# Kernel tuning notes

Measured on AMD Instinct MI355X. Metric: run time of the kernel, lower is better.

## Reference

```python
import jax, jax.numpy as jnp
import numpy as np
from jax import lax

B, S, E, DF, H, L, V, T = 32, 512, 512, 2048, 8, 2, 30000, 12
START, STOP = 10, 11
NEG = -10000.0


def setup_inputs() -> dict:
    key = jax.random.key(0)
    ks = jax.random.split(key, 12)
    g = lambda i, shape, sc=0.02: jax.random.normal(ks[i], shape, jnp.float32) * sc
    trans = jax.random.normal(ks[9], (T, T), jnp.float32)
    trans = trans.at[START, :].set(NEG).at[:, STOP].set(NEG)
    return {
        "sentence": jax.random.randint(ks[0], (B, S), 0, V),
        "seq_len": jax.random.randint(ks[1], (B,), 1, S + 1),
        "tags": jax.random.randint(ks[2], (B, S), 0, 10),
        "emb": g(3, (V, E), 1.0),
        "attn_in_w": g(4, (L, 3 * E, E)), "attn_in_b": jnp.zeros((L, 3 * E)),
        "attn_out_w": g(5, (L, E, E)), "attn_out_b": jnp.zeros((L, E)),
        "ln1_g": jnp.ones((L, E)), "ln1_b": jnp.zeros((L, E)),
        "ln2_g": jnp.ones((L, E)), "ln2_b": jnp.zeros((L, E)),
        "ff1_w": g(6, (L, DF, E)), "ff1_b": jnp.zeros((L, DF)),
        "ff2_w": g(7, (L, E, DF)), "ff2_b": jnp.zeros((L, E)),
        "tag_w": g(8, (T, E)), "tag_b": jnp.zeros((T,)),
        "transitions": trans,
    }


def _ln(x, g, b):
    m = x.mean(-1, keepdims=True)
    v = ((x - m) ** 2).mean(-1, keepdims=True)
    return (x - m) / jnp.sqrt(v + 1e-5) * g + b


def _mha(x, w_in, b_in, w_out, b_out):
    b_, s_, e_ = x.shape
    d = e_ // H
    qkv = x @ w_in.T + b_in
    q, k, v = jnp.split(qkv, 3, axis=-1)
    split = lambda t: t.reshape(b_, s_, H, d).transpose(0, 2, 1, 3)
    q, k, v = split(q), split(k), split(v)
    att = jax.nn.softmax(jnp.einsum('bhqd,bhkd->bhqk', q, k) / np.sqrt(d).astype(np.float32), axis=-1)
    o = jnp.einsum('bhqk,bhkd->bhqd', att, v).transpose(0, 2, 1, 3).reshape(b_, s_, e_)
    return o @ w_out.T + b_out


def _forward_impl(sentence, seq_len, tags, emb, attn_in_w, attn_in_b, attn_out_w,
                  attn_out_b, ln1_g, ln1_b, ln2_g, ln2_b, ff1_w, ff1_b, ff2_w,
                  ff2_b, tag_w, tag_b, transitions):
    # Transformer encoder features (dropout in eval mode -> identity)
    x = emb[sentence]  # (B,S,E)
    for l in range(L):
        x = _ln(x + _mha(x, attn_in_w[l], attn_in_b[l], attn_out_w[l], attn_out_b[l]), ln1_g[l], ln1_b[l])
        h = jax.nn.relu(x @ ff1_w[l].T + ff1_b[l]) @ ff2_w[l].T + ff2_b[l]
        x = _ln(x + h, ln2_g[l], ln2_b[l])
    feats = x @ tag_w.T + tag_b  # (B,S,T)

    # CRF forward algorithm (log-semiring scan, masked by seq_len)
    alpha0 = jnp.full((B, T), NEG, feats.dtype).at[:, START].set(0.0)

    def step(alpha, xs):
        emit_t, t = xs  # emit_t: (B,T)
        new = emit_t + jax.nn.logsumexp(alpha[:, None, :] + transitions[None, :, :], axis=-1)
        return jnp.where((t < seq_len)[:, None], new, alpha), None

    alpha, _ = lax.scan(step, alpha0, (feats.transpose(1, 0, 2), jnp.arange(S)))
    fwd_score = jax.nn.logsumexp(alpha + transitions[STOP][None, :], axis=-1)  # (B,)

    # gold score (vectorized _score_sentence)
    tags_ext = jnp.concatenate([jnp.full((B, 1), START, tags.dtype), tags], axis=1)  # (B,S+1)
    mask = jnp.arange(S)[None, :] < seq_len[:, None]  # (B,S)
    trans_sc = jnp.where(mask, transitions[tags_ext[:, 1:], tags_ext[:, :-1]], 0.0).sum(-1)
    emit_sc = jnp.where(mask, jnp.take_along_axis(feats, tags[:, :, None], axis=2)[..., 0], 0.0).sum(-1)
    last_tag = jnp.take_along_axis(tags_ext, seq_len[:, None], axis=1)[:, 0]
    gold = trans_sc + emit_sc + transitions[STOP, last_tag]

    return jnp.mean(fwd_score - gold)


def reference(sentence, seq_len, tags, emb, attn_in_w, attn_in_b, attn_out_w,
              attn_out_b, ln1_g, ln1_b, ln2_g, ln2_b, ff1_w, ff1_b, ff2_w,
              ff2_b, tag_w, tag_b, transitions):
    return _forward_impl(sentence, seq_len, tags, emb, attn_in_w, attn_in_b,
                         attn_out_w, attn_out_b, ln1_g, ln1_b, ln2_g, ln2_b,
                         ff1_w, ff1_b, ff2_w, ff2_b, tag_w, tag_b, transitions)
```

## Files before the change

kernel.cpp:

```cpp
#include <hip/hip_runtime.h>
#include <hip/hip_bf16.h>

#define BB 32
#define SSZ 512
#define EE 512
#define DFF 2048
#define HH 8
#define LL 2
#define TT 12
#define START_TAG 10
#define STOP_TAG 11
#define CB 8
#define CM (CB * SSZ)
#define NCHUNK (BB / CB)
#define NBH (CB * HH)
#define NBH_ALL (BB * HH)
#define NCHK 8

typedef __hip_bfloat16 bf16;
typedef __attribute__((ext_vector_type(8))) short short8;
typedef __attribute__((ext_vector_type(4))) float f32x4;

__device__ __forceinline__ float b2f(bf16 x) { return __bfloat162float(x); }
__device__ __forceinline__ float ldw(const void* p, size_t i, bool isbf) {
  return isbf ? __bfloat162float(((const bf16*)p)[i]) : ((const float*)p)[i];
}

__device__ __forceinline__ void gl_lds16(const bf16* g, bf16* l) {
  __builtin_amdgcn_global_load_lds(
      (const __attribute__((address_space(1))) void*)g,
      (__attribute__((address_space(3))) void*)l, 16, 0, 0);
}

__device__ __forceinline__ void stg128(const bf16* __restrict__ G, int ldk,
                                       int row0, int col0, bf16* lds0,
                                       int w, int l) {
#pragma unroll
  for (int q = 0; q < 2; ++q) {
    int lr = q * 64 + w * 8 + (l >> 3);
    int gs = (l & 7) ^ (lr & 7);
    gl_lds16(G + (size_t)(row0 + lr) * ldk + col0 + gs * 8,
             lds0 + (q * 64 + w * 8) * 64);
  }
}

__device__ __forceinline__ short8 ldfrag(const bf16* T, int row, int gr) {
  return *(const short8*)&T[row * 64 + ((gr ^ (row & 7)) << 3)];
}

__global__ void k_detect(const void* trans, int* dflag) {
  if (threadIdx.x == 0) {
    const unsigned short* u = (const unsigned short*)trans;
    dflag[0] = (u[START_TAG * TT] == 0xC61C && u[START_TAG * TT + 1] == 0xC61C) ? 1 : 0;
  }
}

__global__ void k_cvt(const void* src, bf16* dst, long n, const int* dflag) {
  bool isbf = dflag[0] != 0;
  for (long i = (long)blockIdx.x * 256 + threadIdx.x; i < n; i += (long)gridDim.x * 256)
    dst[i] = __float2bfloat16(ldw(src, i, isbf));
}

__global__ void k_embed(const int* sent, const void* emb, bf16* xb, const int* dflag) {
  bool isbf = dflag[0] != 0;
  int tok = blockIdx.x;
  int v = sent[tok];
  bf16* xo = xb + (size_t)tok * EE;
  for (int i = threadIdx.x; i < EE; i += 256)
    xo[i] = __float2bfloat16(ldw(emb, (size_t)v * EE + i, isbf));
}

__global__ __launch_bounds__(512, 4) void k_mg128(
    const bf16* __restrict__ A, const bf16* __restrict__ W,
    const void* __restrict__ bias, size_t boff, bf16* __restrict__ Cb,
    bf16* __restrict__ vtout, int M, int N, int K, int relu,
    const int* __restrict__ dflag) {
  constexpr int BUFSZ = 16384;
  extern __shared__ __align__(16) bf16 Sh[];
  const bool isbf = dflag[0] != 0;
  const int tid = threadIdx.x;
  const int l = tid & 63;
  const int w = tid >> 6;
  const int wm = w >> 1, wn = w & 1;
  const int lrow = l & 15, lk = l >> 4;
  const int m0 = blockIdx.x * 128, n0 = blockIdx.y * 128;

  f32x4 acc[2][4];
#pragma unroll
  for (int i = 0; i < 2; ++i)
#pragma unroll
    for (int j = 0; j < 4; ++j) acc[i][j] = (f32x4){0.f, 0.f, 0.f, 0.f};

  const int NT = K >> 6;

#pragma unroll
  for (int p = 0; p < 2; ++p) {
    stg128(A, K, m0, p * 64, Sh + p * BUFSZ, w, l);
    stg128(W, K, n0, p * 64, Sh + p * BUFSZ + 8192, w, l);
  }
  asm volatile("s_waitcnt vmcnt(4)" ::: "memory");
  __builtin_amdgcn_sched_barrier(0);
  __builtin_amdgcn_s_barrier();

#pragma unroll 1
  for (int t = 0; t < NT; ++t) {
    bf16* Ab = Sh + (t & 1) * BUFSZ;
    bf16* Bb = Ab + 8192;
    const bool more = (t + 2 < NT);
    short8 bfr[2][4], a0[2], a1[2];
#pragma unroll
    for (int kb = 0; kb < 2; ++kb) {
#pragma unroll
      for (int nf = 0; nf < 4; ++nf)
        bfr[kb][nf] = ldfrag(Bb, wn * 64 + nf * 16 + lrow, kb * 4 + lk);
      a0[kb] = ldfrag(Ab, wm * 32 + lrow, kb * 4 + lk);
      a1[kb] = ldfrag(Ab, wm * 32 + 16 + lrow, kb * 4 + lk);
    }
    asm volatile("s_waitcnt lgkmcnt(0)" ::: "memory");
    __builtin_amdgcn_sched_barrier(0);
    __builtin_amdgcn_s_barrier();
    __builtin_amdgcn_sched_barrier(0);
    if (more) {
      stg128(A, K, m0, (t + 2) * 64, Ab, w, l);
      stg128(W, K, n0, (t + 2) * 64, Bb, w, l);
    }
    __builtin_amdgcn_s_setprio(1);
#pragma unroll
    for (int kb = 0; kb < 2; ++kb)
#pragma unroll
      for (int nf = 0; nf < 4; ++nf)
        acc[0][nf] = __builtin_amdgcn_mfma_f32_16x16x32_bf16(
            a0[kb], bfr[kb][nf], acc[0][nf], 0, 0, 0);
#pragma unroll
    for (int kb = 0; kb < 2; ++kb)
#pragma unroll
      for (int nf = 0; nf < 4; ++nf)
        acc[1][nf] = __builtin_amdgcn_mfma_f32_16x16x32_bf16(
            a1[kb], bfr[kb][nf], acc[1][nf], 0, 0, 0);
    __builtin_amdgcn_s_setprio(0);
    if (more) asm volatile("s_waitcnt vmcnt(4)" ::: "memory");
    else asm volatile("s_waitcnt vmcnt(0)" ::: "memory");
    __builtin_amdgcn_sched_barrier(0);
    __builtin_amdgcn_s_barrier();
  }

  const bool vpath = (vtout != nullptr) && (n0 >= 1024);
  if (!vpath) {
#pragma unroll
    for (int nf = 0; nf < 4; ++nf) {
      const int c = wn * 64 + nf * 16 + lrow;
      const float bia = ldw(bias, boff + n0 + c, isbf);
#pragma unroll
      for (int mf = 0; mf < 2; ++mf)
#pragma unroll
        for (int r = 0; r < 4; ++r) {
          const int row = wm * 32 + mf * 16 + lk * 4 + r;
          float v = acc[mf][nf][r] + bia;
          if (relu) v = fmaxf(v, 0.f);
          Sh[row * 128 + (c ^ (((row >> 2) & 7) << 4))] = __float2bfloat16(v);
        }
    }
    __syncthreads();
#pragma unroll
    for (int p = 0; p < 4; ++p) {
      const int row = p * 32 + (tid >> 4);
      const int g = tid & 15;
      *(uint4*)(Cb + (size_t)(m0 + row) * N + n0 + g * 8) =
          *(const uint4*)&Sh[row * 128 + ((g * 8) ^ (((row >> 2) & 7) << 4))];
    }
  } else {
    const int pos0 = m0 & 511;
    const int blb = (m0 >> 9) * 8;
#pragma unroll
    for (int nf = 0; nf < 4; ++nf) {
      const int c = wn * 64 + nf * 16 + lrow;
      const float bia = ldw(bias, boff + n0 + c, isbf);
#pragma unroll
      for (int mf = 0; mf < 2; ++mf)
#pragma unroll
        for (int r = 0; r < 4; ++r) {
          const int row = wm * 32 + mf * 16 + lk * 4 + r;
          Sh[c * 128 + (row ^ (((c >> 2) & 7) << 4))] =
              __float2bfloat16(acc[mf][nf][r] + bia);
        }
    }
    __syncthreads();
#pragma unroll
    for (int p = 0; p < 4; ++p) {
      const int cc = p * 32 + (tid >> 4);
      const int g = tid & 15;
      const int vc = n0 - 1024 + cc;
      *(uint4*)(vtout + ((size_t)(blb + (vc >> 6)) * 64 + (vc & 63)) * 512 +
                pos0 + g * 8) =
          *(const uint4*)&Sh[cc * 128 + ((g * 8) ^ (((cc >> 2) & 7) << 4))];
    }
  }
}

#define LDP 72
__global__ __launch_bounds__(512) void k_flash(const bf16* __restrict__ qkv,
                                               const bf16* __restrict__ vt,
                                               bf16* __restrict__ ctx) {
  extern __shared__ __align__(16) bf16 Fs[];
  const int bh = blockIdx.x;
  const int bl = bh >> 3, h = bh & 7;
  const int m0 = blockIdx.y * 256;
  const int tid = threadIdx.x;
  const int l = tid & 63;
  const int w = tid >> 6;
  const int lrow = l & 15, lk = l >> 4;

  bf16* Psw = Fs + 16384 + w * (32 * LDP);

  short8 qf[2][2];
  {
    const bf16* Qb = qkv + (size_t)(bl * SSZ + m0 + w * 32) * 1536 + h * 64;
#pragma unroll
    for (int mf = 0; mf < 2; ++mf)
#pragma unroll
      for (int kb = 0; kb < 2; ++kb)
        qf[mf][kb] = *(const short8*)(Qb + (size_t)(mf * 16 + lrow) * 1536 + kb * 32 + lk * 8);
  }

  f32x4 acc_o[2][4];
  float lsum[2][4];
#pragma unroll
  for (int mf = 0; mf < 2; ++mf) {
#pragma unroll
    for (int nf = 0; nf < 4; ++nf) acc_o[mf][nf] = (f32x4){0.f, 0.f, 0.f, 0.f};
#pragma unroll
    for (int r = 0; r < 4; ++r) lsum[mf][r] = 0.f;
  }

  const int srow = w * 8 + (l >> 3);
  const int gsw = (l & 7) ^ (srow & 7);
  const bf16* Ksrc = qkv + (size_t)(bl * SSZ + srow) * 1536 + 512 + h * 64 + gsw * 8;
  const bf16* Vsrc = vt + ((size_t)bh * 64 + srow) * SSZ + gsw * 8;
#define STAGE_KV(kt, b)                                                       \
  do {                                                                        \
    gl_lds16(Ksrc + (size_t)(kt)*64 * 1536, Fs + (b)*8192 + w * 512);         \
    gl_lds16(Vsrc + (kt)*64, Fs + (b)*8192 + 4096 + w * 512);                 \
  } while (0)

  STAGE_KV(0, 0);
  __syncthreads();

  for (int kt = 0; kt < 8; ++kt) {
    const int cur = kt & 1;
    if (kt < 7) STAGE_KV(kt + 1, cur ^ 1);
    const bf16* Ks = Fs + cur * 8192;
    const bf16* Vs = Ks + 4096;

    f32x4 s[2][4];
#pragma unroll
    for (int mf = 0; mf < 2; ++mf)
#pragma unroll
      for (int nf = 0; nf < 4; ++nf) s[mf][nf] = (f32x4){0.f, 0.f, 0.f, 0.f};
#pragma unroll
    for (int kb = 0; kb < 2; ++kb) {
      short8 bk[4];
#pragma unroll
      for (int nf = 0; nf < 4; ++nf)
        bk[nf] = ldfrag(Ks, nf * 16 + lrow, kb * 4 + lk);
#pragma unroll
      for (int mf = 0; mf < 2; ++mf)
#pragma unroll
        for (int nf = 0; nf < 4; ++nf)
          s[mf][nf] = __builtin_amdgcn_mfma_f32_16x16x32_bf16(qf[mf][kb], bk[nf],
                                                              s[mf][nf], 0, 0, 0);
    }
#pragma unroll
    for (int mf = 0; mf < 2; ++mf)
#pragma unroll
      for (int r = 0; r < 4; ++r) {
        float p0 = __expf(0.125f * s[mf][0][r]);
        float p1 = __expf(0.125f * s[mf][1][r]);
        float p2 = __expf(0.125f * s[mf][2][r]);
        float p3 = __expf(0.125f * s[mf][3][r]);
        s[mf][0][r] = p0; s[mf][1][r] = p1; s[mf][2][r] = p2; s[mf][3][r] = p3;
        lsum[mf][r] += (p0 + p1) + (p2 + p3);
      }
#pragma unroll
    for (int mf = 0; mf < 2; ++mf)
#pragma unroll
      for (int nf = 0; nf < 4; ++nf)
#pragma unroll
        for (int r = 0; r < 4; ++r)
          Psw[(mf * 16 + lk * 4 + r) * LDP + nf * 16 + lrow] =
              __float2bfloat16(s[mf][nf][r]);
#pragma unroll
    for (int kb = 0; kb < 2; ++kb) {
      short8 ap[2], bv[4];
#pragma unroll
      for (int mf = 0; mf < 2; ++mf)
        ap[mf] = *(const short8*)&Psw[(mf * 16 + lrow) * LDP + kb * 32 + lk * 8];
#pragma unroll
      for (int nf = 0; nf < 4; ++nf)
        bv[nf] = ldfrag(Vs, nf * 16 + lrow, kb * 4 + lk);
#pragma unroll
      for (int mf = 0; mf < 2; ++mf)
#pragma unroll
        for (int nf = 0; nf < 4; ++nf)
          acc_o[mf][nf] = __builtin_amdgcn_mfma_f32_16x16x32_bf16(ap[mf], bv[nf],
                                                                  acc_o[mf][nf], 0, 0, 0);
    }
    __syncthreads();
  }
#undef STAGE_KV
#pragma unroll
  for (int mf = 0; mf < 2; ++mf) {
#pragma unroll
    for (int r = 0; r < 4; ++r) {
      float ls = lsum[mf][r];
      ls += __shfl_xor(ls, 1, 64);
      ls += __shfl_xor(ls, 2, 64);
      ls += __shfl_xor(ls, 4, 64);
      ls += __shfl_xor(ls, 8, 64);
      float inv = 1.f / ls;
      int q = m0 + w * 32 + mf * 16 + lk * 4 + r;
#pragma unroll
      for (int nf = 0; nf < 4; ++nf)
        ctx[((size_t)(bl * SSZ + q)) * EE + h * 64 + nf * 16 + lrow] =
            __float2bfloat16(acc_o[mf][nf][r] * inv);
    }
  }
}

__global__ void k_ln_res(bf16* xb, const bf16* hb, const void* g,
                         const void* be, size_t goff, const int* dflag) {
  bool isbf = dflag[0] != 0;
  int tok = blockIdx.x, tid = threadIdx.x;
  size_t base = (size_t)tok * EE;
  float v0 = b2f(xb[base + tid]) + b2f(hb[base + tid]);
  float v1 = b2f(xb[base + tid + 256]) + b2f(hb[base + tid + 256]);
  float s = v0 + v1, ss = v0 * v0 + v1 * v1;
#pragma unroll
  for (int off = 32; off > 0; off >>= 1) {
    s += __shfl_down(s, off, 64);
    ss += __shfl_down(ss, off, 64);
  }
  __shared__ float ps[4], pss[4];
  __shared__ float mean_s, rstd_s;
  int w = tid >> 6;
  if ((tid & 63) == 0) { ps[w] = s; pss[w] = ss; }
  __syncthreads();
  if (tid == 0) {
    float S_ = ps[0] + ps[1] + ps[2] + ps[3];
    float SS_ = pss[0] + pss[1] + pss[2] + pss[3];
    float mu = S_ / (float)EE;
    float var = SS_ / (float)EE - mu * mu;
    mean_s = mu;
    rstd_s = rsqrtf(var + 1e-5f);
  }
  __syncthreads();
  float mu = mean_s, rs = rstd_s;
  float r0 = (v0 - mu) * rs * ldw(g, goff + tid, isbf) + ldw(be, goff + tid, isbf);
  float r1 = (v1 - mu) * rs * ldw(g, goff + tid + 256, isbf) + ldw(be, goff + tid + 256, isbf);
  xb[base + tid] = __float2bfloat16(r0);
  xb[base + tid + 256] = __float2bfloat16(r1);
}

__global__ void k_feats(const bf16* xb, const bf16* tgw, const void* tgb,
                        float* feats, const int* dflag) {
  bool isbf = dflag[0] != 0;
  int m = blockIdx.x * 4 + (threadIdx.x >> 6);
  int lane = threadIdx.x & 63;
  uint4 raw = *(const uint4*)(xb + (size_t)m * EE + lane * 8);
  const bf16* rb = (const bf16*)&raw;
  float xv[8];
#pragma unroll
  for (int j = 0; j < 8; ++j) xv[j] = b2f(rb[j]);
#pragma unroll
  for (int t = 0; t < TT; ++t) {
    uint4 wraw = *(const uint4*)(tgw + t * EE + lane * 8);
    const bf16* wb = (const bf16*)&wraw;
    float s = 0.f;
#pragma unroll
    for (int j = 0; j < 8; ++j) s += xv[j] * b2f(wb[j]);
#pragma unroll
    for (int off = 32; off > 0; off >>= 1) s += __shfl_down(s, off, 64);
    if (lane == 0) feats[(size_t)m * TT + t] = s + ldw(tgb, t, isbf);
  }
}

__global__ void k_crf1(const float* feats, const int* seq_len, const void* trans_in,
                       float* cmat, const int* dflag) {
  bool isbf = dflag[0] != 0;
  int c = blockIdx.x, b = blockIdx.y;
  int tid = threadIdx.x;
  __shared__ float tr[144];
  __shared__ float abuf[2][144];
  if (tid < 144) tr[tid] = ldw(trans_in, tid, isbf);
  bool act = tid < 144;
  int i = tid / 12, j = tid % 12;
  if (act) abuf[0][tid] = (i == j) ? 0.f : -1e30f;
  __syncthreads();
  float trrow[12];
  if (act) {
#pragma unroll
    for (int k = 0; k < 12; ++k) trrow[k] = tr[i * 12 + k];
  }
  int len = seq_len[b];
  int t0 = c * 64;
  int t1 = min(len, t0 + 64);
  int cur = 0;
  for (int t = t0; t < t1; ++t) {
    float nv = 0.f;
    if (act) {
      float m = -1e30f, v[12];
#pragma unroll
      for (int k = 0; k < 12; ++k) {
        v[k] = trrow[k] + abuf[cur][k * 12 + j];
        m = fmaxf(m, v[k]);
      }
      float s = 0.f;
#pragma unroll
      for (int k = 0; k < 12; ++k) s += __expf(v[k] - m);
      nv = feats[((size_t)b * SSZ + t) * TT + i] + m + __logf(s);
    }
    if (act) abuf[cur ^ 1][tid] = nv;
    __syncthreads();
    cur ^= 1;
  }
  if (act) cmat[((size_t)b * NCHK + c) * 144 + tid] = abuf[cur][tid];
}

__global__ void k_crf2(const float* cmat, const float* feats, const int* tags,
                       const int* seq_len, const void* trans_in, float* bscore,
                       const int* dflag) {
  bool isbf = dflag[0] != 0;
  int b = blockIdx.x;
  int tid = threadIdx.x;
  __shared__ float tr[144];
  __shared__ float tbuf[2][144];
  __shared__ float alpha_sh[12];
  if (tid < 144) tr[tid] = ldw(trans_in, tid, isbf);
  bool act = tid < 144;
  int i = tid / 12, j = tid % 12;
  if (act) tbuf[0][tid] = cmat[((size_t)b * NCHK) * 144 + tid];
  __syncthreads();
  int cur = 0;
  for (int c = 1; c < NCHK; ++c) {
    float nv = 0.f;
    if (act) {
      const float* Cc = cmat + ((size_t)b * NCHK + c) * 144;
      float m = -1e30f, v[12];
#pragma unroll
      for (int k = 0; k < 12; ++k) {
        v[k] = Cc[i * 12 + k] + tbuf[cur][k * 12 + j];
        m = fmaxf(m, v[k]);
      }
      float s = 0.f;
#pragma unroll
      for (int k = 0; k < 12; ++k) s += __expf(v[k] - m);
      nv = m + __logf(s);
    }
    if (act) tbuf[cur ^ 1][tid] = nv;
    __syncthreads();
    cur ^= 1;
  }
  if (tid < 12) {
    float m = -1e30f, v[12];
#pragma unroll
    for (int k = 0; k < 12; ++k) {
      float a0 = (k == START_TAG) ? 0.f : -10000.f;
      v[k] = tbuf[cur][tid * 12 + k] + a0;
      m = fmaxf(m, v[k]);
    }
    float s = 0.f;
#pragma unroll
    for (int k = 0; k < 12; ++k) s += __expf(v[k] - m);
    alpha_sh[tid] = m + __logf(s);
  }
  __syncthreads();
  if (tid < 64) {
    int lane = tid;
    int len = seq_len[b];
    float part = 0.f;
    for (int s = lane; s < len; s += 64) {
      int ct = tags[b * SSZ + s];
      int pv = (s == 0) ? START_TAG : tags[b * SSZ + s - 1];
      part += tr[ct * 12 + pv] + feats[((size_t)b * SSZ + s) * TT + ct];
    }
#pragma unroll
    for (int off = 32; off > 0; off >>= 1) part += __shfl_down(part, off, 64);
    if (lane == 0) {
      float m = -1e30f;
#pragma unroll
      for (int k = 0; k < 12; ++k) m = fmaxf(m, alpha_sh[k] + tr[STOP_TAG * 12 + k]);
      float s = 0.f;
#pragma unroll
      for (int k = 0; k < 12; ++k) s += __expf(alpha_sh[k] + tr[STOP_TAG * 12 + k] - m);
      float fwd = m + __logf(s);
      int last = tags[b * SSZ + len - 1];
      bscore[b] = fwd - (part + tr[STOP_TAG * 12 + last]);
    }
  }
}

__global__ void k_final(const float* bscore, float* out) {
  int tid = threadIdx.x;
  float v = (tid < BB) ? bscore[tid] : 0.f;
#pragma unroll
  for (int off = 32; off > 0; off >>= 1) v += __shfl_down(v, off, 64);
  if (tid == 0) out[0] = v / (float)BB;
}

extern "C" void kernel_launch(void* const* d_in, const int* in_sizes, int n_in,
                              void* d_out, int out_size, void* d_ws, size_t ws_size,
                              hipStream_t stream) {
  const int* sentence = (const int*)d_in[0];
  const int* seq_len = (const int*)d_in[1];
  const int* tags = (const int*)d_in[2];
  const void* emb = d_in[3];
  const void* attn_in_w = d_in[4];
  const void* attn_in_b = d_in[5];
  const void* attn_out_w = d_in[6];
  const void* attn_out_b = d_in[7];
  const void* ln1_g = d_in[8];
  const void* ln1_b = d_in[9];
  const void* ln2_g = d_in[10];
  const void* ln2_b = d_in[11];
  const void* ff1_w = d_in[12];
  const void* ff1_b = d_in[13];
  const void* ff2_w = d_in[14];
  const void* ff2_b = d_in[15];
  const void* tag_w = d_in[16];
  const void* tag_b = d_in[17];
  const void* transitions = d_in[18];

  static int attr_done = 0;
  if (!attr_done) {
    (void)hipFuncSetAttribute((const void*)&k_mg128,
                              hipFuncAttributeMaxDynamicSharedMemorySize, 65536);
    (void)hipFuncSetAttribute((const void*)&k_flash,
                              hipFuncAttributeMaxDynamicSharedMemorySize, 131072);
    attr_done = 1;
  }
  const int GLDS = 65536;
  const int FLDS = (16384 + 8 * 32 * LDP) * 2;

  const int M = BB * SSZ;
  const size_t WEL = (size_t)LL * 3 * EE * EE + (size_t)LL * EE * EE +
                     (size_t)LL * DFF * EE + (size_t)LL * EE * DFF + (size_t)TT * EE;

  size_t o = 0;
  size_t f_feats = o; o += (size_t)M * TT;
  size_t f_bsc = o; o += 64;
  size_t f_cmat = o; o += (size_t)BB * NCHK * 144;
  size_t f_dflag = o; o += 16;
  size_t f_xb = o; o += (size_t)M * EE / 2;
  size_t f_hb = o; o += (size_t)M * EE / 2;
  size_t f_ctxb = o; o += (size_t)M * EE / 2;
  size_t f_act = o; o += (size_t)M * DFF / 2;
  size_t f_vt = o; o += (size_t)NBH_ALL * 64 * SSZ / 2;
  size_t f_w = o; o += (WEL + 1) / 2 + 8;
  size_t need_full = o * 4;
  bool full = ws_size >= need_full;

  float* ws = (float*)d_ws;
  if (full) {
    float* feats = ws + f_feats;
    float* bsc = ws + f_bsc;
    float* cmat = ws + f_cmat;
    int* dflag = (int*)(ws + f_dflag);
    bf16* xb = (bf16*)(ws + f_xb);
    bf16* hb = (bf16*)(ws + f_hb);
    bf16* ctxb = (bf16*)(ws + f_ctxb);
    bf16* act = (bf16*)(ws + f_act);
    bf16* vt = (bf16*)(ws + f_vt);
    bf16* w_aiw = (bf16*)(ws + f_w);
    bf16* w_aow = w_aiw + (size_t)LL * 3 * EE * EE;
    bf16* w_f1 = w_aow + (size_t)LL * EE * EE;
    bf16* w_f2 = w_f1 + (size_t)LL * DFF * EE;
    bf16* w_tg = w_f2 + (size_t)LL * EE * DFF;

    k_detect<<<dim3(1), dim3(64), 0, stream>>>(transitions, dflag);
    k_cvt<<<dim3(1024), dim3(256), 0, stream>>>(attn_in_w, w_aiw, (long)LL * 3 * EE * EE, dflag);
    k_cvt<<<dim3(512), dim3(256), 0, stream>>>(attn_out_w, w_aow, (long)LL * EE * EE, dflag);
    k_cvt<<<dim3(1024), dim3(256), 0, stream>>>(ff1_w, w_f1, (long)LL * DFF * EE, dflag);
    k_cvt<<<dim3(1024), dim3(256), 0, stream>>>(ff2_w, w_f2, (long)LL * EE * DFF, dflag);
    k_cvt<<<dim3(24), dim3(256), 0, stream>>>(tag_w, w_tg, (long)TT * EE, dflag);
    k_embed<<<dim3(M), dim3(256), 0, stream>>>(sentence, emb, xb, dflag);

    for (int l = 0; l < LL; ++l) {
      k_mg128<<<dim3(M / 128, 12), dim3(512), GLDS, stream>>>(
          xb, w_aiw + (size_t)l * 3 * EE * EE, attn_in_b, (size_t)l * 3 * EE,
          act, vt, M, 3 * EE, EE, 0, dflag);
      k_flash<<<dim3(NBH_ALL, 2), dim3(512), FLDS, stream>>>(act, vt, ctxb);
      k_mg128<<<dim3(M / 128, 4), dim3(512), GLDS, stream>>>(
          ctxb, w_aow + (size_t)l * EE * EE, attn_out_b, (size_t)l * EE,
          hb, (bf16*)nullptr, M, EE, EE, 0, dflag);
      k_ln_res<<<dim3(M), dim3(256), 0, stream>>>(xb, hb, ln1_g, ln1_b,
                                                  (size_t)l * EE, dflag);
      k_mg128<<<dim3(M / 128, 16), dim3(512), GLDS, stream>>>(
          xb, w_f1 + (size_t)l * DFF * EE, ff1_b, (size_t)l * DFF,
          act, (bf16*)nullptr, M, DFF, EE, 1, dflag);
      k_mg128<<<dim3(M / 128, 4), dim3(512), GLDS, stream>>>(
          act, w_f2 + (size_t)l * EE * DFF, ff2_b, (size_t)l * EE,
          hb, (bf16*)nullptr, M, EE, DFF, 0, dflag);
      k_ln_res<<<dim3(M), dim3(256), 0, stream>>>(xb, hb, ln2_g, ln2_b,
                                                  (size_t)l * EE, dflag);
    }
    k_feats<<<dim3(M / 4), dim3(256), 0, stream>>>(xb, w_tg, tag_b, feats, dflag);
    k_crf1<<<dim3(NCHK, BB), dim3(192), 0, stream>>>(feats, seq_len, transitions, cmat, dflag);
    k_crf2<<<dim3(BB), dim3(192), 0, stream>>>(cmat, feats, tags, seq_len, transitions, bsc, dflag);
    k_final<<<dim3(1), dim3(64), 0, stream>>>(bsc, (float*)d_out);
  } else {
    float* feats = ws;
    float* bsc = feats + (size_t)M * TT;
    float* cmat = bsc + 64;
    int* dflag = (int*)(cmat + (size_t)BB * NCHK * 144 + 16);
    bf16* xb = (bf16*)(dflag + 16);
    bf16* hb = xb + (size_t)M * EE;
    bf16* qkvb = hb + (size_t)CM * EE;
    bf16* ctxb = qkvb + (size_t)CM * 1536;
    bf16* ffh = ctxb + (size_t)CM * EE;
    bf16* vt = ffh + (size_t)CM * DFF;
    bf16* w_aiw = vt + (size_t)NBH * 64 * SSZ;
    bf16* w_aow = w_aiw + (size_t)LL * 3 * EE * EE;
    bf16* w_f1 = w_aow + (size_t)LL * EE * EE;
    bf16* w_f2 = w_f1 + (size_t)LL * DFF * EE;
    bf16* w_tg = w_f2 + (size_t)LL * EE * DFF;

    k_detect<<<dim3(1), dim3(64), 0, stream>>>(transitions, dflag);
    k_cvt<<<dim3(1024), dim3(256), 0, stream>>>(attn_in_w, w_aiw, (long)LL * 3 * EE * EE, dflag);
    k_cvt<<<dim3(512), dim3(256), 0, stream>>>(attn_out_w, w_aow, (long)LL * EE * EE, dflag);
    k_cvt<<<dim3(1024), dim3(256), 0, stream>>>(ff1_w, w_f1, (long)LL * DFF * EE, dflag);
    k_cvt<<<dim3(1024), dim3(256), 0, stream>>>(ff2_w, w_f2, (long)LL * EE * DFF, dflag);
    k_cvt<<<dim3(24), dim3(256), 0, stream>>>(tag_w, w_tg, (long)TT * EE, dflag);
    k_embed<<<dim3(M), dim3(256), 0, stream>>>(sentence, emb, xb, dflag);

    for (int l = 0; l < LL; ++l) {
      for (int c = 0; c < NCHUNK; ++c) {
        bf16* xbc = xb + (size_t)c * CM * EE;
        k_mg128<<<dim3(CM / 128, 12), dim3(512), GLDS, stream>>>(
            xbc, w_aiw + (size_t)l * 3 * EE * EE, attn_in_b, (size_t)l * 3 * EE,
            qkvb, vt, CM, 3 * EE, EE, 0, dflag);
        k_flash<<<dim3(NBH, 2), dim3(512), FLDS, stream>>>(qkvb, vt, ctxb);
        k_mg128<<<dim3(CM / 128, 4), dim3(512), GLDS, stream>>>(
            ctxb, w_aow + (size_t)l * EE * EE, attn_out_b, (size_t)l * EE,
            hb, (bf16*)nullptr, CM, EE, EE, 0, dflag);
        k_ln_res<<<dim3(CM), dim3(256), 0, stream>>>(xbc, hb, ln1_g, ln1_b,
                                                     (size_t)l * EE, dflag);
        k_mg128<<<dim3(CM / 128, 16), dim3(512), GLDS, stream>>>(
            xbc, w_f1 + (size_t)l * DFF * EE, ff1_b, (size_t)l * DFF,
            ffh, (bf16*)nullptr, CM, DFF, EE, 1, dflag);
        k_mg128<<<dim3(CM / 128, 4), dim3(512), GLDS, stream>>>(
            ffh, w_f2 + (size_t)l * EE * DFF, ff2_b, (size_t)l * EE,
            hb, (bf16*)nullptr, CM, EE, DFF, 0, dflag);
        k_ln_res<<<dim3(CM), dim3(256), 0, stream>>>(xbc, hb, ln2_g, ln2_b,
                                                     (size_t)l * EE, dflag);
      }
    }
    k_feats<<<dim3(M / 4), dim3(256), 0, stream>>>(xb, w_tg, tag_b, feats, dflag);
    k_crf1<<<dim3(NCHK, BB), dim3(192), 0, stream>>>(feats, seq_len, transitions, cmat, dflag);
    k_crf2<<<dim3(BB), dim3(192), 0, stream>>>(cmat, feats, tags, seq_len, transitions, bsc, dflag);
    k_final<<<dim3(1), dim3(64), 0, stream>>>(bsc, (float*)d_out);
  }
}
```

Before: 673.9 us.

## Rework GEMM to 256-thread blocks with 64x64 warp tiles and simpler double buffering

The 128x128 GEMM tile now runs with 4 waves instead of 8, so each wave computes a 64x64 subtile with 16 accumulators and reuses each A/B fragment across more MFMAs. The pipeline moves from a 2-ahead prefetch with manual vmcnt waits to a 1-ahead double buffer synchronised with __syncthreads. The V-transpose epilogue writes 4-element vectors to LDS. In exchange, per-thread register pressure and the number of staging loads per thread both grow, and the shallower prefetch can expose more global-load latency.

```diff
diff --git a/kernel.cpp b/kernel.cpp
--- a/kernel.cpp
+++ b/kernel.cpp
@@ -32,20 +32,12 @@
       (__attribute__((address_space(3))) void*)l, 16, 0, 0);
 }
 
-__device__ __forceinline__ void stg128(const bf16* __restrict__ G, int ldk,
-                                       int row0, int col0, bf16* lds0,
-                                       int w, int l) {
-#pragma unroll
-  for (int q = 0; q < 2; ++q) {
-    int lr = q * 64 + w * 8 + (l >> 3);
-    int gs = (l & 7) ^ (lr & 7);
-    gl_lds16(G + (size_t)(row0 + lr) * ldk + col0 + gs * 8,
-             lds0 + (q * 64 + w * 8) * 64);
-  }
-}
-
 __device__ __forceinline__ short8 ldfrag(const bf16* T, int row, int gr) {
   return *(const short8*)&T[row * 64 + ((gr ^ (row & 7)) << 3)];
+}
+
+__device__ __forceinline__ int swz(int row, int col) {
+  return row * 128 + (col ^ (((row >> 2) & 7) * 16));
 }
 
 __global__ void k_detect(const void* trans, int* dflag) {
@@ -70,12 +62,11 @@
     xo[i] = __float2bfloat16(ldw(emb, (size_t)v * EE + i, isbf));
 }
 
-__global__ __launch_bounds__(512, 4) void k_mg128(
+__global__ __launch_bounds__(256, 2) void k_mg128(
     const bf16* __restrict__ A, const bf16* __restrict__ W,
     const void* __restrict__ bias, size_t boff, bf16* __restrict__ Cb,
     bf16* __restrict__ vtout, int M, int N, int K, int relu,
     const int* __restrict__ dflag) {
-  constexpr int BUFSZ = 16384;
   extern __shared__ __align__(16) bf16 Sh[];
   const bool isbf = dflag[0] != 0;
   const int tid = threadIdx.x;
@@ -85,114 +76,116 @@
   const int lrow = l & 15, lk = l >> 4;
   const int m0 = blockIdx.x * 128, n0 = blockIdx.y * 128;
 
-  f32x4 acc[2][4];
-#pragma unroll
-  for (int i = 0; i < 2; ++i)
+  const int srow = w * 8 + (l >> 3);
+  const bf16* aS[4];
+  const bf16* bS[4];
+#pragma unroll
+  for (int q = 0; q < 4; ++q) {
+    int r = q * 32 + srow;
+    int gs = (l & 7) ^ (r & 7);
+    aS[q] = A + (size_t)(m0 + r) * K + gs * 8;
+    bS[q] = W + (size_t)(n0 + r) * K + gs * 8;
+  }
+
+  f32x4 acc[4][4];
+#pragma unroll
+  for (int i = 0; i < 4; ++i)
 #pragma unroll
     for (int j = 0; j < 4; ++j) acc[i][j] = (f32x4){0.f, 0.f, 0.f, 0.f};
 
   const int NT = K >> 6;
 
-#pragma unroll
-  for (int p = 0; p < 2; ++p) {
-    stg128(A, K, m0, p * 64, Sh + p * BUFSZ, w, l);
-    stg128(W, K, n0, p * 64, Sh + p * BUFSZ + 8192, w, l);
-  }
-  asm volatile("s_waitcnt vmcnt(4)" ::: "memory");
-  __builtin_amdgcn_sched_barrier(0);
-  __builtin_amdgcn_s_barrier();
+#define STG(t, buf)                                                       \
+  do {                                                                    \
+    bf16* dA = Sh + (buf)*16384;                                          \
+    bf16* dB = dA + 8192;                                                 \
+    _Pragma("unroll") for (int q = 0; q < 4; ++q) {                       \
+      gl_lds16(aS[q] + (t)*64, dA + (q * 32 + w * 8) * 64);               \
+      gl_lds16(bS[q] + (t)*64, dB + (q * 32 + w * 8) * 64);               \
+    }                                                                     \
+  } while (0)
+
+  STG(0, 0);
+  __syncthreads();
 
 #pragma unroll 1
   for (int t = 0; t < NT; ++t) {
-    bf16* Ab = Sh + (t & 1) * BUFSZ;
-    bf16* Bb = Ab + 8192;
-    const bool more = (t + 2 < NT);
-    short8 bfr[2][4], a0[2], a1[2];
-#pragma unroll
-    for (int kb = 0; kb < 2; ++kb) {
+    if (t + 1 < NT) STG(t + 1, (t + 1) & 1);
+    __builtin_amdgcn_sched_barrier(0);
+    const bf16* Ab = Sh + (t & 1) * 16384;
+    const bf16* Bb = Ab + 8192;
+    short8 af[4][2], bq[4][2];
+#pragma unroll
+    for (int f = 0; f < 4; ++f)
+#pragma unroll
+      for (int kb = 0; kb < 2; ++kb) {
+        af[f][kb] = ldfrag(Ab, wm * 64 + f * 16 + lrow, kb * 4 + lk);
+        bq[f][kb] = ldfrag(Bb, wn * 64 + f * 16 + lrow, kb * 4 + lk);
+      }
+    __builtin_amdgcn_s_setprio(1);
+#pragma unroll
+    for (int mf = 0; mf < 4; ++mf)
 #pragma unroll
       for (int nf = 0; nf < 4; ++nf)
-        bfr[kb][nf] = ldfrag(Bb, wn * 64 + nf * 16 + lrow, kb * 4 + lk);
-      a0[kb] = ldfrag(Ab, wm * 32 + lrow, kb * 4 + lk);
-      a1[kb] = ldfrag(Ab, wm * 32 + 16 + lrow, kb * 4 + lk);
-    }
-    asm volatile("s_waitcnt lgkmcnt(0)" ::: "memory");
-    __builtin_amdgcn_sched_barrier(0);
-    __builtin_amdgcn_s_barrier();
-    __builtin_amdgcn_sched_barrier(0);
-    if (more) {
-      stg128(A, K, m0, (t + 2) * 64, Ab, w, l);
-      stg128(W, K, n0, (t + 2) * 64, Bb, w, l);
-    }
-    __builtin_amdgcn_s_setprio(1);
-#pragma unroll
-    for (int kb = 0; kb < 2; ++kb)
-#pragma unroll
-      for (int nf = 0; nf < 4; ++nf)
-        acc[0][nf] = __builtin_amdgcn_mfma_f32_16x16x32_bf16(
-            a0[kb], bfr[kb][nf], acc[0][nf], 0, 0, 0);
-#pragma unroll
-    for (int kb = 0; kb < 2; ++kb)
-#pragma unroll
-      for (int nf = 0; nf < 4; ++nf)
-        acc[1][nf] = __builtin_amdgcn_mfma_f32_16x16x32_bf16(
-            a1[kb], bfr[kb][nf], acc[1][nf], 0, 0, 0);
+#pragma unroll
+        for (int kb = 0; kb < 2; ++kb)
+          acc[mf][nf] = __builtin_amdgcn_mfma_f32_16x16x32_bf16(
+              af[mf][kb], bq[nf][kb], acc[mf][nf], 0, 0, 0);
     __builtin_amdgcn_s_setprio(0);
-    if (more) asm volatile("s_waitcnt vmcnt(4)" ::: "memory");
-    else asm volatile("s_waitcnt vmcnt(0)" ::: "memory");
-    __builtin_amdgcn_sched_barrier(0);
-    __builtin_amdgcn_s_barrier();
-  }
+    __syncthreads();
+  }
+#undef STG
 
   const bool vpath = (vtout != nullptr) && (n0 >= 1024);
   if (!vpath) {
 #pragma unroll
     for (int nf = 0; nf < 4; ++nf) {
-      const int c = wn * 64 + nf * 16 + lrow;
-      const float bia = ldw(bias, boff + n0 + c, isbf);
-#pragma unroll
-      for (int mf = 0; mf < 2; ++mf)
+      int nl = wn * 64 + nf * 16 + lrow;
+      float bia = ldw(bias, boff + n0 + nl, isbf);
+#pragma unroll
+      for (int mf = 0; mf < 4; ++mf) {
 #pragma unroll
         for (int r = 0; r < 4; ++r) {
-          const int row = wm * 32 + mf * 16 + lk * 4 + r;
+          int ml = wm * 64 + mf * 16 + lk * 4 + r;
           float v = acc[mf][nf][r] + bia;
           if (relu) v = fmaxf(v, 0.f);
-          Sh[row * 128 + (c ^ (((row >> 2) & 7) << 4))] = __float2bfloat16(v);
+          Sh[swz(ml, nl)] = __float2bfloat16(v);
         }
+      }
     }
     __syncthreads();
 #pragma unroll
-    for (int p = 0; p < 4; ++p) {
-      const int row = p * 32 + (tid >> 4);
-      const int g = tid & 15;
-      *(uint4*)(Cb + (size_t)(m0 + row) * N + n0 + g * 8) =
-          *(const uint4*)&Sh[row * 128 + ((g * 8) ^ (((row >> 2) & 7) << 4))];
+    for (int p = 0; p < 8; ++p) {
+      int row = p * 16 + (tid >> 4);
+      int off = (tid & 15) * 8;
+      *(uint4*)(Cb + (size_t)(m0 + row) * N + n0 + off) =
+          *(const uint4*)&Sh[swz(row, off)];
     }
   } else {
-    const int pos0 = m0 & 511;
-    const int blb = (m0 >> 9) * 8;
 #pragma unroll
     for (int nf = 0; nf < 4; ++nf) {
-      const int c = wn * 64 + nf * 16 + lrow;
-      const float bia = ldw(bias, boff + n0 + c, isbf);
-#pragma unroll
-      for (int mf = 0; mf < 2; ++mf)
-#pragma unroll
-        for (int r = 0; r < 4; ++r) {
-          const int row = wm * 32 + mf * 16 + lk * 4 + r;
-          Sh[c * 128 + (row ^ (((c >> 2) & 7) << 4))] =
-              __float2bfloat16(acc[mf][nf][r] + bia);
-        }
+      int nl = wn * 64 + nf * 16 + lrow;
+      float bia = ldw(bias, boff + n0 + nl, isbf);
+#pragma unroll
+      for (int mf = 0; mf < 4; ++mf) {
+        int mlb = wm * 64 + mf * 16 + lk * 4;
+        bf16 t4[4];
+#pragma unroll
+        for (int r = 0; r < 4; ++r) t4[r] = __float2bfloat16(acc[mf][nf][r] + bia);
+        *(uint2*)&Sh[swz(nl, mlb)] = *(const uint2*)t4;
+      }
     }
     __syncthreads();
-#pragma unroll
-    for (int p = 0; p < 4; ++p) {
-      const int cc = p * 32 + (tid >> 4);
-      const int g = tid & 15;
-      const int vc = n0 - 1024 + cc;
-      *(uint4*)(vtout + ((size_t)(blb + (vc >> 6)) * 64 + (vc & 63)) * 512 +
-                pos0 + g * 8) =
-          *(const uint4*)&Sh[cc * 128 + ((g * 8) ^ (((cc >> 2) & 7) << 4))];
+    int h0 = (n0 - 1024) >> 6;
+    int blb = (m0 >> 9) * 8;
+    int pos0 = m0 & 511;
+#pragma unroll
+    for (int p = 0; p < 8; ++p) {
+      int drow = p * 16 + (tid >> 4);
+      int poff = (tid & 15) * 8;
+      bf16* dst = vtout + ((size_t)(blb + h0 + (drow >> 6)) * 64 + (drow & 63)) * 512 +
+                  pos0 + poff;
+      *(uint4*)dst = *(const uint4*)&Sh[swz(drow, poff)];
     }
   }
 }
@@ -584,19 +577,19 @@
     k_embed<<<dim3(M), dim3(256), 0, stream>>>(sentence, emb, xb, dflag);
 
     for (int l = 0; l < LL; ++l) {
-      k_mg128<<<dim3(M / 128, 12), dim3(512), GLDS, stream>>>(
+      k_mg128<<<dim3(M / 128, 12), dim3(256), GLDS, stream>>>(
           xb, w_aiw + (size_t)l * 3 * EE * EE, attn_in_b, (size_t)l * 3 * EE,
           act, vt, M, 3 * EE, EE, 0, dflag);
       k_flash<<<dim3(NBH_ALL, 2), dim3(512), FLDS, stream>>>(act, vt, ctxb);
-      k_mg128<<<dim3(M / 128, 4), dim3(512), GLDS, stream>>>(
+      k_mg128<<<dim3(M / 128, 4), dim3(256), GLDS, stream>>>(
           ctxb, w_aow + (size_t)l * EE * EE, attn_out_b, (size_t)l * EE,
           hb, (bf16*)nullptr, M, EE, EE, 0, dflag);
       k_ln_res<<<dim3(M), dim3(256), 0, stream>>>(xb, hb, ln1_g, ln1_b,
                                                   (size_t)l * EE, dflag);
-      k_mg128<<<dim3(M / 128, 16), dim3(512), GLDS, stream>>>(
+      k_mg128<<<dim3(M / 128, 16), dim3(256), GLDS, stream>>>(
           xb, w_f1 + (size_t)l * DFF * EE, ff1_b, (size_t)l * DFF,
           act, (bf16*)nullptr, M, DFF, EE, 1, dflag);
-      k_mg128<<<dim3(M / 128, 4), dim3(512), GLDS, stream>>>(
+      k_mg128<<<dim3(M / 128, 4), dim3(256), GLDS, stream>>>(
           act, w_f2 + (size_t)l * EE * DFF, ff2_b, (size_t)l * EE,
           hb, (bf16*)nullptr, M, EE, DFF, 0, dflag);
       k_ln_res<<<dim3(M), dim3(256), 0, stream>>>(xb, hb, ln2_g, ln2_b,
@@ -634,19 +627,19 @@
     for (int l = 0; l < LL; ++l) {
       for (int c = 0; c < NCHUNK; ++c) {
         bf16* xbc = xb + (size_t)c * CM * EE;
-        k_mg128<<<dim3(CM / 128, 12), dim3(512), GLDS, stream>>>(
+        k_mg128<<<dim3(CM / 128, 12), dim3(256), GLDS, stream>>>(
             xbc, w_aiw + (size_t)l * 3 * EE * EE, attn_in_b, (size_t)l * 3 * EE,
             qkvb, vt, CM, 3 * EE, EE, 0, dflag);
         k_flash<<<dim3(NBH, 2), dim3(512), FLDS, stream>>>(qkvb, vt, ctxb);
-        k_mg128<<<dim3(CM / 128, 4), dim3(512), GLDS, stream>>>(
+        k_mg128<<<dim3(CM / 128, 4), dim3(256), GLDS, stream>>>(
             ctxb, w_aow + (size_t)l * EE * EE, attn_out_b, (size_t)l * EE,
             hb, (bf16*)nullptr, CM, EE, EE, 0, dflag);
         k_ln_res<<<dim3(CM), dim3(256), 0, stream>>>(xbc, hb, ln1_g, ln1_b,
                                                      (size_t)l * EE, dflag);
-        k_mg128<<<dim3(CM / 128, 16), dim3(512), GLDS, stream>>>(
+        k_mg128<<<dim3(CM / 128, 16), dim3(256), GLDS, stream>>>(
             xbc, w_f1 + (size_t)l * DFF * EE, ff1_b, (size_t)l * DFF,
             ffh, (bf16*)nullptr, CM, DFF, EE, 1, dflag);
-        k_mg128<<<dim3(CM / 128, 4), dim3(512), GLDS, stream>>>(
+        k_mg128<<<dim3(CM / 128, 4), dim3(256), GLDS, stream>>>(
             ffh, w_f2 + (size_t)l * EE * DFF, ff2_b, (size_t)l * EE,
             hb, (bf16*)nullptr, CM, EE, DFF, 0, dflag);
         k_ln_res<<<dim3(CM), dim3(256), 0, stream>>>(xbc, hb, ln2_g, ln2_b,
```

After: 666.1 us. Within noise of the previous version (-1.2%).
